# Optimization experiments

Hardware: AMD Instinct MI355X
Metric: run time of the kernel (lower is better)

Reference implementation:

```python
import jax, jax.numpy as jnp
import numpy as np

# Output shape from ToDenseMink.__init__:
#   batch=4, out_size=256, x = 512 // (2//1) = 256, y = 512 // (2//1) = 256
B, C, X, Y = 4, 256, 256, 256
N = 200000  # number of occupied sparse cells


def setup_inputs() -> dict:
    key = jax.random.key(0)
    kf, kc = jax.random.split(key)
    feats = jax.random.normal(kf, (N, C), dtype=jnp.float32)
    # Unique (batch, x, y) coordinates so the scatter is well-defined
    # (MinkowskiEngine sparse tensors have unique coordinates).
    lin = jax.random.permutation(kc, B * X * Y)[:N]
    b = lin // (X * Y)
    rem = lin % (X * Y)
    x = rem // Y
    y = rem % Y
    coords = jnp.stack([b, x, y], axis=-1).astype(jnp.int32)  # [N, 3]
    return {"feats": feats, "coords": coords}


def reference(feats, coords):
    # Equivalent of x.dense(shape=[B, C, X, Y], min_coordinate=0)[0]:
    # scatter each feature row into the dense grid at (batch, :, x, y).
    dense = jnp.zeros((B, C, X, Y), dtype=feats.dtype)
    dense = dense.at[coords[:, 0], :, coords[:, 1], coords[:, 2]].set(
        feats, mode="drop"
    )
    return dense
```

## Files before the change

kernel.cpp:

```cpp
#include <hip/hip_runtime.h>

#define BB 4
#define CC 256
#define XX 256
#define YY 256
#define NCELLS (BB * XX * YY)

__global__ void k_fill_idx(int4* __restrict__ idx4) {
    int i = blockIdx.x * blockDim.x + threadIdx.x;
    idx4[i] = make_int4(-1, -1, -1, -1);
}

__global__ void k_scatter_idx(const int* __restrict__ coords,
                              int* __restrict__ idx, int n) {
    int i = blockIdx.x * blockDim.x + threadIdx.x;
    if (i >= n) return;
    int b = coords[i * 3 + 0];
    int x = coords[i * 3 + 1];
    int y = coords[i * 3 + 2];
    if ((unsigned)b < BB && (unsigned)x < XX && (unsigned)y < YY) {
        idx[(b * XX + x) * YY + y] = i;
    }
}

__global__ void k_gather_out(const float4* __restrict__ feats4,
                             const int* __restrict__ idx,
                             float* __restrict__ out) {
    int bx = blockIdx.x;
    int y  = threadIdx.x;
    int b  = bx >> 8;
    int x  = bx & 255;

    int row = idx[bx * YY + y];
    bool valid = (row >= 0);
    const float4* fr = feats4 + (size_t)(valid ? row : 0) * (CC / 4);

    float* outp = out + ((size_t)b * CC * XX + x) * YY + y;

    #pragma unroll 4
    for (int c4 = 0; c4 < CC / 4; ++c4) {
        float4 v = fr[c4];
        if (!valid) { v.x = 0.f; v.y = 0.f; v.z = 0.f; v.w = 0.f; }
        int o = (c4 * 4) * (XX * YY);
        outp[o]               = v.x;
        outp[o + XX * YY]     = v.y;
        outp[o + 2 * XX * YY] = v.z;
        outp[o + 3 * XX * YY] = v.w;
    }
}

extern "C" void kernel_launch(void* const* d_in, const int* in_sizes, int n_in,
                              void* d_out, int out_size, void* d_ws, size_t ws_size,
                              hipStream_t stream) {
    const float* feats  = (const float*)d_in[0];
    const int*   coords = (const int*)d_in[1];
    int n = in_sizes[1] / 3;

    int*   idx   = (int*)d_ws;
    float* out   = (float*)d_out;

    k_fill_idx<<<NCELLS / 4 / 256, 256, 0, stream>>>((int4*)idx);

    k_scatter_idx<<<(n + 255) / 256, 256, 0, stream>>>(coords, idx, n);

    k_gather_out<<<BB * XX, 256, 0, stream>>>((const float4*)feats, idx, out);
}
```

Measured before the change: 415.8 us.

## Transpose feature rows through shared memory tiles for coalesced gather and store

Each block now handles 32 y-cells of one (b,x) row. Wavefronts load whole feature rows with coalesced float4 reads into a padded LDS tile, then write channel-major float4 outputs after a barrier. This targets the uncoalesced per-thread row reads of the old gather kernel. It adds an LDS round trip and shorter contiguous write segments (128B per channel).

```diff
diff --git a/kernel.cpp b/kernel.cpp
--- a/kernel.cpp
+++ b/kernel.cpp
@@ -5,6 +5,9 @@
 #define XX 256
 #define YY 256
 #define NCELLS (BB * XX * YY)
+
+#define TILE_Y 32
+#define C_PAD  260
 
 __global__ void k_fill_idx(int4* __restrict__ idx4) {
     int i = blockIdx.x * blockDim.x + threadIdx.x;
@@ -23,29 +26,57 @@
     }
 }
 
+__launch_bounds__(256)
 __global__ void k_gather_out(const float4* __restrict__ feats4,
                              const int* __restrict__ idx,
                              float* __restrict__ out) {
-    int bx = blockIdx.x;
-    int y  = threadIdx.x;
-    int b  = bx >> 8;
-    int x  = bx & 255;
+    __shared__ float tile[TILE_Y][C_PAD];
 
-    int row = idx[bx * YY + y];
-    bool valid = (row >= 0);
-    const float4* fr = feats4 + (size_t)(valid ? row : 0) * (CC / 4);
+    int blk = blockIdx.x;
+    int b   = blk >> 11;
+    int x   = (blk >> 3) & 255;
+    int y0  = (blk & 7) * TILE_Y;
 
-    float* outp = out + ((size_t)b * CC * XX + x) * YY + y;
+    int t    = threadIdx.x;
+    int lane = t & 63;
+    int wv   = t >> 6;
 
-    #pragma unroll 4
-    for (int c4 = 0; c4 < CC / 4; ++c4) {
-        float4 v = fr[c4];
-        if (!valid) { v.x = 0.f; v.y = 0.f; v.z = 0.f; v.w = 0.f; }
-        int o = (c4 * 4) * (XX * YY);
-        outp[o]               = v.x;
-        outp[o + XX * YY]     = v.y;
-        outp[o + 2 * XX * YY] = v.z;
-        outp[o + 3 * XX * YY] = v.w;
+    int cellbase = (b * XX + x) * YY + y0;
+    int iv = idx[cellbase + (lane & 31)];
+
+    int rows[8];
+    #pragma unroll
+    for (int j = 0; j < 8; ++j)
+        rows[j] = __shfl(iv, wv * 8 + j);
+
+    float4 v[8];
+    #pragma unroll
+    for (int j = 0; j < 8; ++j) {
+        int r = rows[j];
+        if (r >= 0) v[j] = feats4[(size_t)r * (CC / 4) + lane];
+        else        v[j] = make_float4(0.f, 0.f, 0.f, 0.f);
+    }
+
+    #pragma unroll
+    for (int j = 0; j < 8; ++j) {
+        int cell = wv * 8 + j;
+        *(float4*)&tile[cell][lane * 4] = v[j];
+    }
+    __syncthreads();
+
+    int y4 = t & 7;
+    int cp = t >> 3;
+    size_t outbase = ((size_t)b * CC) * (XX * YY) + (size_t)x * YY + y0 + y4 * 4;
+
+    #pragma unroll
+    for (int p = 0; p < 8; ++p) {
+        int c = p * 32 + cp;
+        float4 o;
+        o.x = tile[y4 * 4 + 0][c];
+        o.y = tile[y4 * 4 + 1][c];
+        o.z = tile[y4 * 4 + 2][c];
+        o.w = tile[y4 * 4 + 3][c];
+        *(float4*)&out[outbase + (size_t)c * (XX * YY)] = o;
     }
 }
 
@@ -56,12 +87,11 @@
     const int*   coords = (const int*)d_in[1];
     int n = in_sizes[1] / 3;
 
-    int*   idx   = (int*)d_ws;
-    float* out   = (float*)d_out;
+    int*   idx = (int*)d_ws;
+    float* out = (float*)d_out;
 
     k_fill_idx<<<NCELLS / 4 / 256, 256, 0, stream>>>((int4*)idx);
-
     k_scatter_idx<<<(n + 255) / 256, 256, 0, stream>>>(coords, idx, n);
-
-    k_gather_out<<<BB * XX, 256, 0, stream>>>((const float4*)feats, idx, out);
+    k_gather_out<<<BB * XX * (YY / TILE_Y), 256, 0, stream>>>(
+        (const float4*)feats, idx, out);
 }
```

New measurement: 416.0 us. No clear change (+0.0%).
